# Kernel tuning notes

Measured on AMD Instinct MI355X. Metric: run time of the kernel, lower is better.

## Reference

```python
import jax, jax.numpy as jnp
import numpy as np

N = 40000        # num nodes
E = 640000       # num edges
F_IN = 512
F_OUT = 32
HEADS = 8
NEG_SLOPE = 0.2
EPS = 1e-16


def setup_inputs() -> dict:
    key = jax.random.key(0)
    k1, k2, k3, k4, k5 = jax.random.split(key, 5)
    x = jax.random.normal(k1, (N, F_IN), dtype=jnp.float32)
    edge_index = jax.random.randint(k2, (2, E), 0, N, dtype=jnp.int32)
    # xavier-uniform-like init scales
    lim_W = float(np.sqrt(6.0 / (F_IN + F_OUT)))
    lim_a = float(np.sqrt(6.0 / (HEADS + F_OUT)))
    W = jax.random.uniform(k3, (HEADS, F_IN, F_OUT), dtype=jnp.float32, minval=-lim_W, maxval=lim_W)
    a_src = jax.random.uniform(k4, (HEADS, F_OUT), dtype=jnp.float32, minval=-lim_a, maxval=lim_a)
    a_dst = jax.random.uniform(k5, (HEADS, F_OUT), dtype=jnp.float32, minval=-lim_a, maxval=lim_a)
    bias = jnp.zeros((HEADS * F_OUT,), dtype=jnp.float32)
    return {"x": x, "edge_index": edge_index, "W": W, "a_src": a_src, "a_dst": a_dst, "bias": bias}


def reference(x, edge_index, W, a_src, a_dst, bias):
    src, dst = edge_index[0], edge_index[1]
    # per-head projection: [N, H, F_out]
    h = jnp.einsum('nd,hdf->nhf', x, W)
    # attention logit pieces computed per-node then gathered per-edge
    # (same math as gathering h then dotting with a)
    s_src = jnp.einsum('nhf,hf->nh', h, a_src)   # [N, H]
    s_dst = jnp.einsum('nhf,hf->nh', h, a_dst)   # [N, H]
    e = s_src[src] + s_dst[dst]                  # [E, H]
    e = jnp.where(e >= 0, e, NEG_SLOPE * e)      # LeakyReLU(0.2)
    # edge softmax over incoming edges of each dst node (global max shift, as in source)
    e = e - jnp.max(e)
    exp_e = jnp.exp(e)
    denom = jax.ops.segment_sum(exp_e, dst, num_segments=N)   # [N, H]
    alpha = exp_e / (denom[dst] + EPS)                        # [E, H]
    # weighted message aggregation (dropout is identity in eval / p=0)
    msg = alpha[..., None] * h[src]                           # [E, H, F_out]
    out = jax.ops.segment_sum(msg, dst, num_segments=N)       # [N, H, F_out]
    out = out.reshape(N, HEADS * F_OUT) + bias                # concat=True
    return out
```

## Files before the change

### kernel.cpp

```cpp
#include <hip/hip_runtime.h>
#include <hip/hip_bf16.h>
#include <math.h>
#include <stdint.h>

#define N_NODES 40000
#define N_EDGES 640000
#define F_IN    512
#define F_OUT   32
#define HEADS   8
#define C_OUT   (HEADS * F_OUT)
#define NEG_SLOPE 0.2f
#define EPS_F   1e-16f
#define MAXDEG  64

typedef __attribute__((ext_vector_type(8)))  short  short8;
typedef __attribute__((ext_vector_type(4)))  short  short4v;
typedef __attribute__((ext_vector_type(16))) float  float16v;

__device__ __forceinline__ void splitT(float f, unsigned short& hi, unsigned short& lo) {
    unsigned u = __float_as_uint(f);
    hi = (unsigned short)(u >> 16);
    float r = f - __uint_as_float(u & 0xFFFF0000u);
    lo = (unsigned short)(__float_as_uint(r) >> 16);
}

__device__ __forceinline__ unsigned short f2bf(float f) {
    unsigned u = __float_as_uint(f);
    return (unsigned short)((u + 0x7FFF + ((u >> 16) & 1)) >> 16);
}

__global__ __launch_bounds__(256) void pack_zero(const float* __restrict__ W,
                                                 unsigned short* __restrict__ Bp,
                                                 int* __restrict__ cursor) {
    if (blockIdx.x < 512) {
        int tid = blockIdx.x * 256 + threadIdx.x;
        int j    = tid & 7;
        int L    = (tid >> 3) & 63;
        int ni   = (tid >> 9) & 1;
        int ktg  = (tid >> 10) & 31;
        int wc   = tid >> 15;
        int k    = ktg * 16 + (L >> 5) * 8 + j;
        int col  = wc * 64 + ni * 32 + (L & 31);
        int hh = col >> 5, f = col & 31;
        Bp[tid] = f2bf(W[hh * (F_IN * F_OUT) + k * F_OUT + f]);
    } else {
        int i = (blockIdx.x - 512) * 256 + threadIdx.x;
        if (i < N_NODES / 4)
            *(int4*)&cursor[i * 4] = (int4){0, 0, 0, 0};
    }
}

#define AS 66
#define GEMM_BLOCKS 1250

__global__ __launch_bounds__(512, 4) void gemm_scatter(const float* __restrict__ x,
                                                       const unsigned short* __restrict__ Bp,
                                                       const float* __restrict__ a_src,
                                                       const float* __restrict__ a_dst,
                                                       unsigned short* __restrict__ h16,
                                                       float* __restrict__ s_src,
                                                       float* __restrict__ s_dst,
                                                       const int* __restrict__ src,
                                                       const int* __restrict__ dst,
                                                       int* __restrict__ cursor,
                                                       int* __restrict__ src_buf) {
    if (blockIdx.x >= GEMM_BLOCKS) {
        int e = (blockIdx.x - GEMM_BLOCKS) * 512 + threadIdx.x;
        int s = src[e], d = dst[e];
        int pos = atomicAdd(&cursor[d], 1);
        if (pos < MAXDEG) src_buf[d * MAXDEG + pos] = s;
        return;
    }

    __shared__ unsigned short As_hi[32 * AS];
    __shared__ unsigned short As_lo[32 * AS];

    const int t = threadIdx.x;
    const int wc = t >> 6, L = t & 63;
    const int r31 = L & 31, half = L >> 5;
    const int n0 = blockIdx.x * 32;

    float16v accH, accL;
#pragma unroll
    for (int r = 0; r < 16; ++r) { accH[r] = 0.f; accL[r] = 0.f; }

    const int kcol = (t & 15) * 4;
    const int rbase = t >> 4;
    const float* xp = &x[(size_t)(n0 + rbase) * F_IN + kcol];

    const unsigned short* bp =
        &Bp[((((size_t)(wc >> 1) * 32) * 2 + (wc & 1)) * 64 + L) * 8];

    float4 stg = *(const float4*)(xp);

#pragma unroll
    for (int st = 0; st < 8; ++st) {
        short8 breg[4];
#pragma unroll
        for (int kt = 0; kt < 4; ++kt)
            breg[kt] = *(const short8*)(bp + (size_t)(st * 4 + kt) * 1024);

        float4 nstg;
        if (st < 7) nstg = *(const float4*)(xp + (st + 1) * 64);

        {
            unsigned short h0, h1, h2, h3, l0, l1, l2, l3;
            splitT(stg.x, h0, l0); splitT(stg.y, h1, l1);
            splitT(stg.z, h2, l2); splitT(stg.w, h3, l3);
            int off = rbase * AS + kcol;
            *(short4v*)&As_hi[off] = (short4v){(short)h0, (short)h1, (short)h2, (short)h3};
            *(short4v*)&As_lo[off] = (short4v){(short)l0, (short)l1, (short)l2, (short)l3};
        }
        __syncthreads();

#pragma unroll
        for (int kt = 0; kt < 4; ++kt) {
            int off = r31 * AS + kt * 16 + half * 8;
            short8 ah = *(const short8*)&As_hi[off];
            short8 al = *(const short8*)&As_lo[off];
            accH = __builtin_amdgcn_mfma_f32_32x32x16_bf16(ah, breg[kt], accH, 0, 0, 0);
            accL = __builtin_amdgcn_mfma_f32_32x32x16_bf16(al, breg[kt], accL, 0, 0, 0);
        }
        __syncthreads();
        stg = nstg;
    }

#pragma unroll
    for (int r = 0; r < 16; ++r) accH[r] += accL[r];

    const int colb = wc * 32 + r31;
#pragma unroll
    for (int r = 0; r < 16; ++r) {
        int row = n0 + (r & 3) + 8 * (r >> 2) + 4 * half;
        h16[(size_t)row * C_OUT + colb] = f2bf(accH[r]);
    }

    {
        float af = a_src[wc * 32 + r31];
        float df = a_dst[wc * 32 + r31];
#pragma unroll
        for (int r = 0; r < 16; ++r) {
            float v = accH[r];
            float vs = v * af;
            float vd = v * df;
#pragma unroll
            for (int m = 1; m < 32; m <<= 1) {
                vs += __shfl_xor(vs, m, 64);
                vd += __shfl_xor(vd, m, 64);
            }
            if (r31 == 0) {
                int row = n0 + (r & 3) + 8 * (r >> 2) + 4 * half;
                s_src[row * 8 + wc] = vs;
                s_dst[row * 8 + wc] = vd;
            }
        }
    }
}

__global__ __launch_bounds__(256) void aggregate(const int* __restrict__ src_buf,
                                                 const unsigned short* __restrict__ h16,
                                                 const float* __restrict__ s_src,
                                                 const float* __restrict__ s_dst,
                                                 const int* __restrict__ cursor,
                                                 const float* __restrict__ bias,
                                                 float* __restrict__ out) {
    const int t = threadIdx.x;
    const int wave = t >> 6, lane = t & 63;
    const int wgid = blockIdx.x * 4 + wave;
    const int ch0 = lane * 4;
    const int hh = lane >> 3;

    auto bf2f = [](short v) { return __uint_as_float(((unsigned)(unsigned short)v) << 16); };
    const float4 b4 = *(const float4*)&bias[ch0];

    for (int n = wgid; n < N_NODES; n += 8192) {
        const int start = n * MAXDEG;
        const int cnt = cursor[n];
        const float sd = s_dst[n * 8 + hh];

        float a0 = 0.f, a1 = 0.f, a2 = 0.f, a3 = 0.f, den = 0.f;

        int base = 0;
        for (; base + 8 <= cnt; base += 8) {
            int idx = start + base;
            int s[8];
#pragma unroll
            for (int u = 0; u < 8; ++u)
                s[u] = src_buf[idx + u];

            short4v v[8];
#pragma unroll
            for (int u = 0; u < 8; ++u)
                v[u] = *(const short4v*)&h16[(size_t)s[u] * C_OUT + ch0];

            float w[8];
#pragma unroll
            for (int u = 0; u < 8; ++u) {
                float e = s_src[s[u] * 8 + hh] + sd;
                e = e >= 0.f ? e : NEG_SLOPE * e;
                w[u] = __expf(e);
            }

#pragma unroll
            for (int u = 0; u < 8; ++u) {
                a0 += w[u] * bf2f(v[u][0]);
                a1 += w[u] * bf2f(v[u][1]);
                a2 += w[u] * bf2f(v[u][2]);
                a3 += w[u] * bf2f(v[u][3]);
                den += w[u];
            }
        }

        int rem = cnt - base;
        if (rem > 0) {
            int idx = start + base;
            int s[8];
#pragma unroll
            for (int u = 0; u < 8; ++u)
                s[u] = (u < rem) ? src_buf[idx + u] : 0;

            short4v v[8];
#pragma unroll
            for (int u = 0; u < 8; ++u)
                v[u] = *(const short4v*)&h16[(size_t)s[u] * C_OUT + ch0];

            float w[8];
#pragma unroll
            for (int u = 0; u < 8; ++u) {
                float e = s_src[s[u] * 8 + hh] + sd;
                e = e >= 0.f ? e : NEG_SLOPE * e;
                w[u] = (u < rem) ? __expf(e) : 0.f;
            }

#pragma unroll
            for (int u = 0; u < 8; ++u) {
                a0 += w[u] * bf2f(v[u][0]);
                a1 += w[u] * bf2f(v[u][1]);
                a2 += w[u] * bf2f(v[u][2]);
                a3 += w[u] * bf2f(v[u][3]);
                den += w[u];
            }
        }

        float inv = 1.0f / (den + EPS_F);
        float4 o;
        o.x = a0 * inv + b4.x;
        o.y = a1 * inv + b4.y;
        o.z = a2 * inv + b4.z;
        o.w = a3 * inv + b4.w;
        *(float4*)&out[(size_t)n * C_OUT + ch0] = o;
    }
}

extern "C" void kernel_launch(void* const* d_in, const int* in_sizes, int n_in,
                              void* d_out, int out_size, void* d_ws, size_t ws_size,
                              hipStream_t stream) {
    const float* x     = (const float*)d_in[0];
    const int*   eidx  = (const int*)d_in[1];
    const float* W     = (const float*)d_in[2];
    const float* a_src = (const float*)d_in[3];
    const float* a_dst = (const float*)d_in[4];
    const float* bias  = (const float*)d_in[5];
    float* out = (float*)d_out;

    const int* src = eidx;
    const int* dst = eidx + N_EDGES;

    char* p = (char*)d_ws;
    auto carve = [&](size_t bytes) {
        char* r = p;
        p += (bytes + 255) & ~(size_t)255;
        return r;
    };
    unsigned short* h16 = (unsigned short*)carve((size_t)N_NODES * C_OUT * 2);
    float* s_src      = (float*)carve((size_t)N_NODES * HEADS * 4);
    float* s_dst      = (float*)carve((size_t)N_NODES * HEADS * 4);
    int*   src_buf    = (int*)carve((size_t)N_NODES * MAXDEG * 4);
    int*   cursor     = (int*)carve((size_t)N_NODES * 4);
    unsigned short* Bp = (unsigned short*)carve((size_t)131072 * 2);

    pack_zero<<<552, 256, 0, stream>>>(W, Bp, cursor);
    gemm_scatter<<<GEMM_BLOCKS + N_EDGES / 512, 512, 0, stream>>>(
        x, Bp, a_src, a_dst, h16, s_src, s_dst, src, dst, cursor, src_buf);
    aggregate<<<2048, 256, 0, stream>>>(src_buf, h16, s_src, s_dst,
                                        cursor, bias, out);
}
```

Measured before the change: 248.4 us.

## Double-buffer GEMM LDS tiles, reorder scatter blocks, share edge weights via shuffles

The GEMM's shared-memory A tiles become double-buffered, with a barrier that waits only on LDS traffic, so the next tile's conversion and store overlap the MFMA work and each step needs one barrier instead of two. The scatter blocks now come first in the grid so edge bucketing is dispatched before the GEMM blocks. In aggregate, each lane computes the exp weight for one edge of its head group and the other lanes fetch it by shuffle, removing eight redundant s_src loads and exps per lane. The cost is twice the LDS per block and extra cross-lane shuffle traffic.

```diff
diff --git a/kernel.cpp b/kernel.cpp
--- a/kernel.cpp
+++ b/kernel.cpp
@@ -28,6 +28,8 @@
     unsigned u = __float_as_uint(f);
     return (unsigned short)((u + 0x7FFF + ((u >> 16) & 1)) >> 16);
 }
+
+#define BARRIER_NOVM() asm volatile("s_waitcnt lgkmcnt(0)\n\ts_barrier" ::: "memory")
 
 __global__ __launch_bounds__(256) void pack_zero(const float* __restrict__ W,
                                                  unsigned short* __restrict__ Bp,
@@ -51,6 +53,7 @@
 }
 
 #define AS 66
+#define SCAT_BLOCKS 1250
 #define GEMM_BLOCKS 1250
 
 __global__ __launch_bounds__(512, 4) void gemm_scatter(const float* __restrict__ x,
@@ -64,21 +67,21 @@
                                                        const int* __restrict__ dst,
                                                        int* __restrict__ cursor,
                                                        int* __restrict__ src_buf) {
-    if (blockIdx.x >= GEMM_BLOCKS) {
-        int e = (blockIdx.x - GEMM_BLOCKS) * 512 + threadIdx.x;
+    if (blockIdx.x < SCAT_BLOCKS) {
+        int e = blockIdx.x * 512 + threadIdx.x;
         int s = src[e], d = dst[e];
         int pos = atomicAdd(&cursor[d], 1);
         if (pos < MAXDEG) src_buf[d * MAXDEG + pos] = s;
         return;
     }
 
-    __shared__ unsigned short As_hi[32 * AS];
-    __shared__ unsigned short As_lo[32 * AS];
+    __shared__ unsigned short As_hi[2][32 * AS];
+    __shared__ unsigned short As_lo[2][32 * AS];
 
     const int t = threadIdx.x;
     const int wc = t >> 6, L = t & 63;
     const int r31 = L & 31, half = L >> 5;
-    const int n0 = blockIdx.x * 32;
+    const int n0 = (blockIdx.x - SCAT_BLOCKS) * 32;
 
     float16v accH, accL;
 #pragma unroll
@@ -91,39 +94,49 @@
     const unsigned short* bp =
         &Bp[((((size_t)(wc >> 1) * 32) * 2 + (wc & 1)) * 64 + L) * 8];
 
-    float4 stg = *(const float4*)(xp);
+#define CONVW(b, s0) do {                                                      \
+        unsigned short h0,h1,h2,h3,l0,l1,l2,l3;                                \
+        splitT((s0).x,h0,l0); splitT((s0).y,h1,l1);                            \
+        splitT((s0).z,h2,l2); splitT((s0).w,h3,l3);                            \
+        int off_ = rbase*AS + kcol;                                            \
+        *(short4v*)&As_hi[b][off_] =                                           \
+            (short4v){(short)h0,(short)h1,(short)h2,(short)h3};                \
+        *(short4v*)&As_lo[b][off_] =                                           \
+            (short4v){(short)l0,(short)l1,(short)l2,(short)l3};                \
+    } while (0)
+
+    float4 stgB = *(const float4*)(xp);
+    CONVW(0, stgB);
+    stgB = *(const float4*)(xp + 64);
+    BARRIER_NOVM();
 
 #pragma unroll
     for (int st = 0; st < 8; ++st) {
+        const int cur = st & 1, nxt = cur ^ 1;
+
         short8 breg[4];
 #pragma unroll
         for (int kt = 0; kt < 4; ++kt)
             breg[kt] = *(const short8*)(bp + (size_t)(st * 4 + kt) * 1024);
 
-        float4 nstg;
-        if (st < 7) nstg = *(const float4*)(xp + (st + 1) * 64);
-
-        {
-            unsigned short h0, h1, h2, h3, l0, l1, l2, l3;
-            splitT(stg.x, h0, l0); splitT(stg.y, h1, l1);
-            splitT(stg.z, h2, l2); splitT(stg.w, h3, l3);
-            int off = rbase * AS + kcol;
-            *(short4v*)&As_hi[off] = (short4v){(short)h0, (short)h1, (short)h2, (short)h3};
-            *(short4v*)&As_lo[off] = (short4v){(short)l0, (short)l1, (short)l2, (short)l3};
-        }
-        __syncthreads();
+        float4 stgC = stgB;
+        if (st < 6) stgC = *(const float4*)(xp + (st + 2) * 64);
+
+        if (st < 7) CONVW(nxt, stgB);
 
 #pragma unroll
         for (int kt = 0; kt < 4; ++kt) {
             int off = r31 * AS + kt * 16 + half * 8;
-            short8 ah = *(const short8*)&As_hi[off];
-            short8 al = *(const short8*)&As_lo[off];
+            short8 ah = *(const short8*)&As_hi[cur][off];
+            short8 al = *(const short8*)&As_lo[cur][off];
             accH = __builtin_amdgcn_mfma_f32_32x32x16_bf16(ah, breg[kt], accH, 0, 0, 0);
             accL = __builtin_amdgcn_mfma_f32_32x32x16_bf16(al, breg[kt], accL, 0, 0, 0);
         }
-        __syncthreads();
-        stg = nstg;
-    }
+
+        if (st < 7) BARRIER_NOVM();
+        stgB = stgC;
+    }
+#undef CONVW
 
 #pragma unroll
     for (int r = 0; r < 16; ++r) accH[r] += accL[r];
@@ -169,6 +182,8 @@
     const int wgid = blockIdx.x * 4 + wave;
     const int ch0 = lane * 4;
     const int hh = lane >> 3;
+    const int eL = lane & 7;
+    const int gbase = lane & 56;
 
     auto bf2f = [](short v) { return __uint_as_float(((unsigned)(unsigned short)v) << 16); };
     const float4 b4 = *(const float4*)&bias[ch0];
@@ -193,13 +208,14 @@
             for (int u = 0; u < 8; ++u)
                 v[u] = *(const short4v*)&h16[(size_t)s[u] * C_OUT + ch0];
 
+            float sc = s_src[s[eL] * 8 + hh] + sd;
+            sc = sc >= 0.f ? sc : NEG_SLOPE * sc;
+            float wx = __expf(sc);
+
             float w[8];
 #pragma unroll
-            for (int u = 0; u < 8; ++u) {
-                float e = s_src[s[u] * 8 + hh] + sd;
-                e = e >= 0.f ? e : NEG_SLOPE * e;
-                w[u] = __expf(e);
-            }
+            for (int u = 0; u < 8; ++u)
+                w[u] = __shfl(wx, gbase | u, 64);
 
 #pragma unroll
             for (int u = 0; u < 8; ++u) {
@@ -224,12 +240,15 @@
             for (int u = 0; u < 8; ++u)
                 v[u] = *(const short4v*)&h16[(size_t)s[u] * C_OUT + ch0];
 
+            float sc = s_src[s[eL] * 8 + hh] + sd;
+            sc = sc >= 0.f ? sc : NEG_SLOPE * sc;
+            float wx = __expf(sc);
+
             float w[8];
 #pragma unroll
             for (int u = 0; u < 8; ++u) {
-                float e = s_src[s[u] * 8 + hh] + sd;
-                e = e >= 0.f ? e : NEG_SLOPE * e;
-                w[u] = (u < rem) ? __expf(e) : 0.f;
+                float ws = __shfl(wx, gbase | u, 64);
+                w[u] = (u < rem) ? ws : 0.f;
             }
 
 #pragma unroll
@@ -280,7 +299,7 @@
     unsigned short* Bp = (unsigned short*)carve((size_t)131072 * 2);
 
     pack_zero<<<552, 256, 0, stream>>>(W, Bp, cursor);
-    gemm_scatter<<<GEMM_BLOCKS + N_EDGES / 512, 512, 0, stream>>>(
+    gemm_scatter<<<SCAT_BLOCKS + GEMM_BLOCKS, 512, 0, stream>>>(
         x, Bp, a_src, a_dst, h16, s_src, s_dst, src, dst, cursor, src_buf);
     aggregate<<<2048, 256, 0, stream>>>(src_buf, h16, s_src, s_dst,
                                         cursor, bias, out);
```

Measured after the change: 264.0 us. 1.06x slower.
